# Optimization experiments

Measured on AMD Instinct MI355X. Metric: run time of the kernel, lower is better.

## Reference

```python
import jax, jax.numpy as jnp
import numpy as np

TEMPERATURE = 0.07
THRESHOLD = 0.7
NUM = 21          # config['data_loader']['args']['class_num']
EPS = 1e-12       # F.normalize eps
NEG_BIG = 1e30


def _nearest_down(x, H, W):
    # torch F.interpolate(mode='nearest'): in_idx = floor(out_idx * in/out)
    Hin, Win = x.shape[-2], x.shape[-1]
    ih = (jnp.arange(H) * Hin) // H
    iw = (jnp.arange(W) * Win) // W
    return x[..., ih[:, None], iw[None, :]]


def _l2n(x):
    return x / jnp.maximum(jnp.linalg.norm(x, axis=1, keepdims=True), EPS)


def setup_inputs() -> dict:
    key = jax.random.key(0)
    ks = jax.random.split(key, 6)
    B, C, H, W = 8, 256, 128, 128
    return {
        "labels": jax.random.randint(ks[0], (B, 512, 512), 0, NUM, dtype=jnp.int64)
        if jax.config.jax_enable_x64 else jax.random.randint(ks[0], (B, 512, 512), 0, NUM, dtype=jnp.int32),
        "features_old": jax.random.normal(ks[1], (B, C, H, W), dtype=jnp.float32),
        "features": jax.random.normal(ks[2], (B, C, H, W), dtype=jnp.float32),
        "outputs_old": jax.random.normal(ks[3], (B, 16, 512, 512), dtype=jnp.float32),
        "outputs": jax.random.normal(ks[4], (B, NUM, 512, 512), dtype=jnp.float32),
        "prototypes": jax.random.normal(ks[5], (NUM, C), dtype=jnp.float32),
        "num_class": 21,
        "num_old_class": 16,
        "num_new_class": 5,
        "epoch": 1,
        "train_step": 1,
        "len_epoch": 100,
    }


def reference(labels, features_old, features, outputs_old, outputs, prototypes,
              num_class, num_old_class, num_new_class, epoch, train_step, len_epoch):
    B, C, H, W = features.shape
    f32 = features.dtype

    # pseudo-label construction
    labels_down = _nearest_down(labels, H, W)                      # [B,H,W] int
    bgr_mask = (labels_down == 0).astype(labels_down.dtype)
    oo = jnp.where(outputs_old < THRESHOLD, 0.0, outputs_old)
    old_pred = jnp.argmax(oo, axis=1)                              # [B,512,512]
    old_down = _nearest_down(old_pred, H, W).astype(labels_down.dtype)
    pseudo = old_down * bgr_mask + labels_down                     # [B,H,W]
    lab = pseudo.reshape(-1)                                       # [N]
    mask = (lab >= 0) & (lab < NUM)

    # [N, C] normalized pixel features
    fa = _l2n(features.transpose(0, 2, 3, 1).reshape(-1, C))
    fo = _l2n(features_old.transpose(0, 2, 3, 1).reshape(-1, C))

    # per-class mean (segment reduce) replacing the python loop over unique labels
    seg = jnp.where(mask, lab, NUM)
    w = mask.astype(f32)
    counts = jax.ops.segment_sum(w, seg, num_segments=NUM + 1)[:NUM]          # [K]
    sum_a = jax.ops.segment_sum(fa * w[:, None], seg, num_segments=NUM + 1)[:NUM]
    sum_o = jax.ops.segment_sum(fo * w[:, None], seg, num_segments=NUM + 1)[:NUM]
    present = counts > 0
    denom = jnp.where(present, counts, 1.0)[:, None]
    anc = jnp.where(present[:, None], sum_a / denom, 0.0)          # [K,C] anchor prototypes
    con_prev = jnp.where(present[:, None], sum_o / denom, 0.0)     # [K,C] old prototypes
    contrast = jax.lax.stop_gradient(jnp.concatenate([anc, con_prev], axis=0))  # [2K,C]

    K = NUM
    eye = jnp.eye(K, dtype=f32)
    rowp = present.astype(f32)                                     # [K]
    colp = jnp.concatenate([rowp, rowp])                           # [2K]
    # labels are unique per row, so R = [I | I]; pos = [0 | I]; neg = 1 - R
    pos_mask = jnp.concatenate([jnp.zeros((K, K), f32), eye], axis=1) * rowp[:, None] * colp[None, :]
    neg_mask = (1.0 - jnp.concatenate([eye, eye], axis=1)) * rowp[:, None] * colp[None, :]

    adc = (anc @ contrast.T) / TEMPERATURE                         # [K,2K]
    # NOTE: faithful to source, negatives use UNshifted logits
    neg = jnp.sum(jnp.exp(adc) * neg_mask, axis=1, keepdims=True)  # [K,1]
    logits_max = jnp.max(jnp.where(colp[None, :] > 0, adc, -NEG_BIG), axis=1, keepdims=True)
    shifted = adc - jax.lax.stop_gradient(logits_max)
    pos_contrast = shifted * pos_mask - jnp.log(jnp.exp(shifted) + neg) * pos_mask

    num = pos_mask.sum(axis=1)
    valid = num > 0
    row_loss = -pos_contrast.sum(axis=1) / jnp.where(valid, num, 1.0)
    loss = jnp.sum(jnp.where(valid, row_loss, 0.0)) / jnp.maximum(jnp.sum(valid.astype(f32)), 1.0)
    return loss
```

## Files before the change

### kernel.cpp

```cpp
#include <hip/hip_runtime.h>
#include <math.h>

#define NPIX   131072
#define CCH    256
#define HW     16384
#define BSTR   4194304
#define NUMC   21
#define KC     5376
#define NREP   16

typedef __attribute__((ext_vector_type(8))) short bf16x8;
typedef __attribute__((ext_vector_type(4))) float f32x4;

static __device__ __forceinline__ uint f2bf(float x) {
    uint u = __builtin_bit_cast(uint, x);
    return (u + 0x7FFFu + ((u >> 16) & 1u)) >> 16;
}
static __device__ __forceinline__ uint ohv(int lbl, int cls, uint iv) {
    return (lbl == cls) ? iv : 0u;
}
static __device__ __forceinline__ float rsq_fast(float x) {
#if __has_builtin(__builtin_amdgcn_rsqf)
    return __builtin_amdgcn_rsqf(x);
#else
    return rsqrtf(x);
#endif
}
static __device__ __forceinline__ uint bfpack_trunc(float x, float y) {
    return __builtin_amdgcn_perm(__builtin_bit_cast(uint, y),
                                 __builtin_bit_cast(uint, x), 0x07060302u);
}

__global__ __launch_bounds__(256) void k_labels(const int* __restrict__ labels,
                                                const float* __restrict__ outputs_old,
                                                int* __restrict__ lab,
                                                float* __restrict__ gcnt)
{
    __shared__ float cnt[NUMC];
    if (threadIdx.x < NUMC) cnt[threadIdx.x] = 0.f;
    __syncthreads();

    int p = blockIdx.x * 256 + threadIdx.x;
    int b = p >> 14;
    int rem = p & 16383;
    int h = rem >> 7;
    int w = rem & 127;
    int ld = labels[b * 262144 + (h * 4) * 512 + (w * 4)];
    int out = ld;
    if (ld == 0) {
        const float* oo = outputs_old + (size_t)b * BSTR + (size_t)(h * 4) * 512 + (w * 4);
        float v0 = oo[0];
        float best = (v0 < 0.7f) ? 0.0f : v0;
        int bi = 0;
        #pragma unroll
        for (int c = 1; c < 16; ++c) {
            float v = oo[(size_t)c * 262144];
            v = (v < 0.7f) ? 0.0f : v;
            if (v > best) { best = v; bi = c; }
        }
        out = bi;
    }
    lab[p] = out;
    unsafeAtomicAdd(&cnt[out], 1.0f);
    __syncthreads();
    if (threadIdx.x < NUMC) unsafeAtomicAdd(&gcnt[threadIdx.x], cnt[threadIdx.x]);
}

__global__ __launch_bounds__(256, 2) void k_msum(const float* __restrict__ fa,
                                                 const float* __restrict__ fo,
                                                 const int* __restrict__ lab,
                                                 float* __restrict__ partA,
                                                 float* __restrict__ partO)
{
    __shared__ ushort tileB[CCH * 128];
    __shared__ float  ssqP[4][128];
    __shared__ float  invnS[128];
    __shared__ int    labS[256];

    const int t = threadIdx.x;
    const int w = t >> 6, l = t & 63;
    const int isO = blockIdx.x & 1;
    const float* __restrict__ src = isO ? fo : fa;
    float* part = isO ? partO : partA;

    const int pbase = (blockIdx.x >> 1) * 256;
    const int img   = pbase >> 14;
    const int hw0   = pbase & 16383;
    const float* g  = src + (size_t)img * BSTR + hw0;

    labS[t] = lab[pbase + t];

    f32x4 acc[2][4];
    #pragma unroll
    for (int m = 0; m < 2; ++m)
        #pragma unroll
        for (int n = 0; n < 4; ++n)
            acc[m][n] = (f32x4){0.f, 0.f, 0.f, 0.f};

#define LOADB(B, i0) do { \
    _Pragma("unroll") \
    for (int i_ = 0; i_ < 8; ++i_) \
        B[i_] = *(const float4*)(gc + (size_t)(w * 64 + 2 * ((i0) + i_) + (l >> 5)) * HW \
                                 + (l & 31) * 4); \
    } while (0)

#define PROCB(B, i0) do { \
    _Pragma("unroll") \
    for (int i_ = 0; i_ < 8; ++i_) { \
        float4 v_ = B[i_]; \
        s4.x += v_.x * v_.x;  s4.y += v_.y * v_.y; \
        s4.z += v_.z * v_.z;  s4.w += v_.w * v_.w; \
        int ch_ = w * 64 + 2 * ((i0) + i_) + (l >> 5); \
        uint lo_ = bfpack_trunc(v_.x, v_.y); \
        uint hi_ = bfpack_trunc(v_.z, v_.w); \
        *(uint2*)((char*)tileB + ch_ * 256 + ((((l & 31) * 8)) ^ ((ch_ & 7) << 4))) = \
            make_uint2(lo_, hi_); \
    } \
    } while (0)

#define KSTEP(c2, ks) do { \
    float4 ivA_ = *(const float4*)&invnS[(ks) * 32 + (l >> 4) * 8]; \
    float4 ivB_ = *(const float4*)&invnS[(ks) * 32 + (l >> 4) * 8 + 4]; \
    uint iv0 = f2bf(ivA_.x), iv1 = f2bf(ivA_.y), iv2 = f2bf(ivA_.z), iv3 = f2bf(ivA_.w); \
    uint iv4 = f2bf(ivB_.x), iv5 = f2bf(ivB_.y), iv6 = f2bf(ivB_.z), iv7 = f2bf(ivB_.w); \
    int4 la_ = *(const int4*)&labS[(c2) * 128 + (ks) * 32 + (l >> 4) * 8]; \
    int4 lb_ = *(const int4*)&labS[(c2) * 128 + (ks) * 32 + (l >> 4) * 8 + 4]; \
    const int cls0_ = l & 15, cls1_ = 16 + (l & 15); \
    uint4 u0_, u1_; \
    u0_.x = ohv(la_.x, cls0_, iv0) | (ohv(la_.y, cls0_, iv1) << 16); \
    u0_.y = ohv(la_.z, cls0_, iv2) | (ohv(la_.w, cls0_, iv3) << 16); \
    u0_.z = ohv(lb_.x, cls0_, iv4) | (ohv(lb_.y, cls0_, iv5) << 16); \
    u0_.w = ohv(lb_.z, cls0_, iv6) | (ohv(lb_.w, cls0_, iv7) << 16); \
    u1_.x = ohv(la_.x, cls1_, iv0) | (ohv(la_.y, cls1_, iv1) << 16); \
    u1_.y = ohv(la_.z, cls1_, iv2) | (ohv(la_.w, cls1_, iv3) << 16); \
    u1_.z = ohv(lb_.x, cls1_, iv4) | (ohv(lb_.y, cls1_, iv5) << 16); \
    u1_.w = ohv(lb_.z, cls1_, iv6) | (ohv(lb_.w, cls1_, iv7) << 16); \
    bf16x8 A0_ = __builtin_bit_cast(bf16x8, u0_); \
    bf16x8 A1_ = __builtin_bit_cast(bf16x8, u1_); \
    _Pragma("unroll") \
    for (int n_ = 0; n_ < 4; ++n_) { \
        const int chrow_ = (w * 4 + n_) * 16 + (l & 15); \
        const bf16x8 B_ = *(const bf16x8*)((const char*)tileB + chrow_ * 256 \
                            + (((ks) * 64 + (l >> 4) * 16) ^ ((chrow_ & 7) << 4))); \
        acc[0][n_] = __builtin_amdgcn_mfma_f32_16x16x32_bf16(A0_, B_, acc[0][n_], 0, 0, 0); \
        acc[1][n_] = __builtin_amdgcn_mfma_f32_16x16x32_bf16(A1_, B_, acc[1][n_], 0, 0, 0); \
    } \
    } while (0)

#define CHUNK(c2, LAST) do { \
    const float* gc = g + (c2) * 128; \
    float4 s4 = {0.f, 0.f, 0.f, 0.f}; \
    float4 bufA[8], bufB[8]; \
    LOADB(bufA, 0);  LOADB(bufB, 8); \
    PROCB(bufA, 0);  LOADB(bufA, 16); \
    PROCB(bufB, 8);  LOADB(bufB, 24); \
    PROCB(bufA, 16); PROCB(bufB, 24); \
    s4.x += __shfl_xor(s4.x, 32, 64);  s4.y += __shfl_xor(s4.y, 32, 64); \
    s4.z += __shfl_xor(s4.z, 32, 64);  s4.w += __shfl_xor(s4.w, 32, 64); \
    if (l < 32) *(float4*)&ssqP[w][l * 4] = s4; \
    __syncthreads(); \
    if (t < 128) { \
        float ss_ = ssqP[0][t] + ssqP[1][t] + ssqP[2][t] + ssqP[3][t]; \
        invnS[t] = rsq_fast(fmaxf(ss_, 1e-24f)); \
    } \
    __syncthreads(); \
    KSTEP(c2, 0); KSTEP(c2, 1); KSTEP(c2, 2); KSTEP(c2, 3); \
    if (!(LAST)) __syncthreads(); \
    } while (0)

    CHUNK(0, 0);
    CHUNK(1, 1);

#undef LOADB
#undef PROCB
#undef KSTEP
#undef CHUNK

    const int rep = (blockIdx.x >> 1) & (NREP - 1);
    #pragma unroll
    for (int m = 0; m < 2; ++m)
        #pragma unroll
        for (int n = 0; n < 4; ++n) {
            const int col = (w * 4 + n) * 16 + (l & 15);
            #pragma unroll
            for (int r = 0; r < 4; ++r) {
                const int row = m * 16 + (l >> 4) * 4 + r;
                if (row < NUMC)
                    unsafeAtomicAdd(&part[rep * KC + row * 256 + col], acc[m][n][r]);
            }
        }
}

__global__ __launch_bounds__(256) void k_red(const float* __restrict__ partA,
                                             const float* __restrict__ partO,
                                             float* __restrict__ gsum)
{
    const int b = blockIdx.x, t = threadIdx.x;
    const float* part = (b < 21) ? partA : partO;
    const int cls = (b < 21) ? b : b - 21;
    float s = 0.f;
    #pragma unroll
    for (int r = 0; r < NREP; ++r) s += part[r * KC + cls * 256 + t];
    gsum[b * 256 + t] = s;
}

__global__ __launch_bounds__(256) void k_final2(const float* __restrict__ gsum,
                                                const float* __restrict__ gcnt,
                                                float* __restrict__ out)
{
    __shared__ float anc[NUMC * 260];
    __shared__ float con[NUMC * 260];
    __shared__ float adc[NUMC * 44];
    __shared__ float cntS[NUMC];
    __shared__ float rowloss[NUMC];
    __shared__ float rowvalid[NUMC];

    if (threadIdx.x < NUMC) cntS[threadIdx.x] = gcnt[threadIdx.x];
    __syncthreads();
    for (int i = threadIdx.x; i < KC; i += 256) {
        int k = i >> 8, c = i & 255;
        float cn = cntS[k];
        bool pr = cn > 0.f;
        float d = pr ? cn : 1.f;
        anc[k * 260 + c] = pr ? gsum[k * 256 + c] / d : 0.f;
        con[k * 260 + c] = pr ? gsum[(NUMC + k) * 256 + c] / d : 0.f;
    }
    __syncthreads();
    for (int pair = threadIdx.x; pair < NUMC * 2 * NUMC; pair += 256) {
        int k = pair / (2 * NUMC);
        int j = pair % (2 * NUMC);
        const float* ar = anc + k * 260;
        const float* br = (j < NUMC) ? (anc + j * 260) : (con + (j - NUMC) * 260);
        float s = 0.f;
        for (int c = 0; c < CCH; c += 4) {
            float4 a4 = *(const float4*)(ar + c);
            float4 b4 = *(const float4*)(br + c);
            s += a4.x * b4.x + a4.y * b4.y + a4.z * b4.z + a4.w * b4.w;
        }
        adc[k * 44 + j] = s / 0.07f;
    }
    __syncthreads();
    if (threadIdx.x < NUMC) {
        int k = threadIdx.x;
        bool pr = cntS[k] > 0.f;
        float neg = 0.f;
        float mx = -1e30f;
        for (int j = 0; j < 2 * NUMC; ++j) {
            int cj = (j < NUMC) ? j : (j - NUMC);
            bool cp = cntS[cj] > 0.f;
            float v = adc[k * 44 + j];
            if (cp) {
                if (v > mx) mx = v;
                if (j != k && j != NUMC + k) neg += expf(v);
            }
        }
        float sh = adc[k * 44 + NUMC + k] - mx;
        float rl = -(sh - logf(expf(sh) + neg));
        rowloss[k] = pr ? rl : 0.f;
        rowvalid[k] = pr ? 1.f : 0.f;
    }
    __syncthreads();
    if (threadIdx.x == 0) {
        float s = 0.f, v = 0.f;
        for (int kk = 0; kk < NUMC; ++kk) { s += rowloss[kk]; v += rowvalid[kk]; }
        out[0] = s / fmaxf(v, 1.f);
    }
}

extern "C" void kernel_launch(void* const* d_in, const int* in_sizes, int n_in,
                              void* d_out, int out_size, void* d_ws, size_t ws_size,
                              hipStream_t stream) {
    const int*   labels      = (const int*)  d_in[0];
    const float* feats_old   = (const float*)d_in[1];
    const float* feats       = (const float*)d_in[2];
    const float* outputs_old = (const float*)d_in[3];

    float* ws    = (float*)d_ws;
    int*   lab   = (int*)ws;
    float* partA = ws + 131072;
    float* partO = partA + NREP * KC;
    float* gcnt  = partO + NREP * KC;
    float* gsum  = gcnt + 32;

    hipMemsetAsync(partA, 0, (size_t)(2 * NREP * KC + NUMC) * sizeof(float), stream);

    k_labels<<<NPIX / 256, 256, 0, stream>>>(labels, outputs_old, lab, gcnt);
    k_msum  <<<1024, 256, 0, stream>>>(feats, feats_old, lab, partA, partO);
    k_red   <<<42, 256, 0, stream>>>(partA, partO, gsum);
    k_final2<<<1, 256, 0, stream>>>(gsum, gcnt, (float*)d_out);
}
```

Before: 101.2 us.

## Process 512 pixels per k_msum block with cross-chunk prefetch and wider loads

Each k_msum block now covers 512 pixels, handled as two 256-pixel halves, and the grid is halved. Each wave loads a full 1 KB channel row per instruction, and the first loads of the second half are issued before the first half's norm and MFMA phase. This is meant to hide load latency and halve the atomic flushes into the partial buffers. In exchange the LDS tile doubles to 128 KB, which forces one block per CU and lowers occupancy. The bf16 packing also moves from truncation to round-to-nearest, which adds ALU work per element.

Measured after the change: 107.8 us. 6.5% more time.

```diff
diff --git a/kernel.cpp b/kernel.cpp
--- a/kernel.cpp
+++ b/kernel.cpp
@@ -25,10 +25,6 @@
 #else
     return rsqrtf(x);
 #endif
-}
-static __device__ __forceinline__ uint bfpack_trunc(float x, float y) {
-    return __builtin_amdgcn_perm(__builtin_bit_cast(uint, y),
-                                 __builtin_bit_cast(uint, x), 0x07060302u);
 }
 
 __global__ __launch_bounds__(256) void k_labels(const int* __restrict__ labels,
@@ -66,16 +62,16 @@
     if (threadIdx.x < NUMC) unsafeAtomicAdd(&gcnt[threadIdx.x], cnt[threadIdx.x]);
 }
 
-__global__ __launch_bounds__(256, 2) void k_msum(const float* __restrict__ fa,
+__global__ __launch_bounds__(256, 1) void k_msum(const float* __restrict__ fa,
                                                  const float* __restrict__ fo,
                                                  const int* __restrict__ lab,
                                                  float* __restrict__ partA,
                                                  float* __restrict__ partO)
 {
-    __shared__ ushort tileB[CCH * 128];
-    __shared__ float  ssqP[4][128];
-    __shared__ float  invnS[128];
-    __shared__ int    labS[256];
+    __shared__ ushort tileB[CCH * 256];
+    __shared__ float  ssqP[4][256];
+    __shared__ float  invnS[256];
+    __shared__ int    labS[512];
 
     const int t = threadIdx.x;
     const int w = t >> 6, l = t & 63;
@@ -83,12 +79,13 @@
     const float* __restrict__ src = isO ? fo : fa;
     float* part = isO ? partO : partA;
 
-    const int pbase = (blockIdx.x >> 1) * 256;
+    const int pbase = (blockIdx.x >> 1) * 512;
     const int img   = pbase >> 14;
     const int hw0   = pbase & 16383;
     const float* g  = src + (size_t)img * BSTR + hw0;
 
-    labS[t] = lab[pbase + t];
+    labS[t]       = lab[pbase + t];
+    labS[256 + t] = lab[pbase + 256 + t];
 
     f32x4 acc[2][4];
     #pragma unroll
@@ -97,34 +94,36 @@
         for (int n = 0; n < 4; ++n)
             acc[m][n] = (f32x4){0.f, 0.f, 0.f, 0.f};
 
-#define LOADB(B, i0) do { \
+#define SWZ(ch_) ((((ch_) & 15) << 4) ^ (((ch_) & 1) << 8))
+
+#define ISSUE(B, su, b) do { \
     _Pragma("unroll") \
     for (int i_ = 0; i_ < 8; ++i_) \
-        B[i_] = *(const float4*)(gc + (size_t)(w * 64 + 2 * ((i0) + i_) + (l >> 5)) * HW \
-                                 + (l & 31) * 4); \
+        B[i_] = *(const float4*)(g + (size_t)(w * 64 + (b) * 8 + i_) * HW \
+                                 + (su) * 256 + 4 * l); \
     } while (0)
 
-#define PROCB(B, i0) do { \
+#define PROC(B, b) do { \
     _Pragma("unroll") \
     for (int i_ = 0; i_ < 8; ++i_) { \
         float4 v_ = B[i_]; \
         s4.x += v_.x * v_.x;  s4.y += v_.y * v_.y; \
         s4.z += v_.z * v_.z;  s4.w += v_.w * v_.w; \
-        int ch_ = w * 64 + 2 * ((i0) + i_) + (l >> 5); \
-        uint lo_ = bfpack_trunc(v_.x, v_.y); \
-        uint hi_ = bfpack_trunc(v_.z, v_.w); \
-        *(uint2*)((char*)tileB + ch_ * 256 + ((((l & 31) * 8)) ^ ((ch_ & 7) << 4))) = \
+        int ch_ = w * 64 + (b) * 8 + i_; \
+        uint lo_ = f2bf(v_.x) | (f2bf(v_.y) << 16); \
+        uint hi_ = f2bf(v_.z) | (f2bf(v_.w) << 16); \
+        *(uint2*)((char*)tileB + ch_ * 512 + ((8 * l) ^ SWZ(ch_))) = \
             make_uint2(lo_, hi_); \
     } \
     } while (0)
 
-#define KSTEP(c2, ks) do { \
+#define KSTEP(su, ks) do { \
     float4 ivA_ = *(const float4*)&invnS[(ks) * 32 + (l >> 4) * 8]; \
     float4 ivB_ = *(const float4*)&invnS[(ks) * 32 + (l >> 4) * 8 + 4]; \
     uint iv0 = f2bf(ivA_.x), iv1 = f2bf(ivA_.y), iv2 = f2bf(ivA_.z), iv3 = f2bf(ivA_.w); \
     uint iv4 = f2bf(ivB_.x), iv5 = f2bf(ivB_.y), iv6 = f2bf(ivB_.z), iv7 = f2bf(ivB_.w); \
-    int4 la_ = *(const int4*)&labS[(c2) * 128 + (ks) * 32 + (l >> 4) * 8]; \
-    int4 lb_ = *(const int4*)&labS[(c2) * 128 + (ks) * 32 + (l >> 4) * 8 + 4]; \
+    int4 la_ = *(const int4*)&labS[(su) * 256 + (ks) * 32 + (l >> 4) * 8]; \
+    int4 lb_ = *(const int4*)&labS[(su) * 256 + (ks) * 32 + (l >> 4) * 8 + 4]; \
     const int cls0_ = l & 15, cls1_ = 16 + (l & 15); \
     uint4 u0_, u1_; \
     u0_.x = ohv(la_.x, cls0_, iv0) | (ohv(la_.y, cls0_, iv1) << 16); \
@@ -140,41 +139,58 @@
     _Pragma("unroll") \
     for (int n_ = 0; n_ < 4; ++n_) { \
         const int chrow_ = (w * 4 + n_) * 16 + (l & 15); \
-        const bf16x8 B_ = *(const bf16x8*)((const char*)tileB + chrow_ * 256 \
-                            + (((ks) * 64 + (l >> 4) * 16) ^ ((chrow_ & 7) << 4))); \
+        const bf16x8 B_ = *(const bf16x8*)((const char*)tileB + chrow_ * 512 \
+                            + (((ks) * 64 + (l >> 4) * 16) ^ SWZ(chrow_))); \
         acc[0][n_] = __builtin_amdgcn_mfma_f32_16x16x32_bf16(A0_, B_, acc[0][n_], 0, 0, 0); \
         acc[1][n_] = __builtin_amdgcn_mfma_f32_16x16x32_bf16(A1_, B_, acc[1][n_], 0, 0, 0); \
     } \
     } while (0)
 
-#define CHUNK(c2, LAST) do { \
-    const float* gc = g + (c2) * 128; \
-    float4 s4 = {0.f, 0.f, 0.f, 0.f}; \
-    float4 bufA[8], bufB[8]; \
-    LOADB(bufA, 0);  LOADB(bufB, 8); \
-    PROCB(bufA, 0);  LOADB(bufA, 16); \
-    PROCB(bufB, 8);  LOADB(bufB, 24); \
-    PROCB(bufA, 16); PROCB(bufB, 24); \
-    s4.x += __shfl_xor(s4.x, 32, 64);  s4.y += __shfl_xor(s4.y, 32, 64); \
-    s4.z += __shfl_xor(s4.z, 32, 64);  s4.w += __shfl_xor(s4.w, 32, 64); \
-    if (l < 32) *(float4*)&ssqP[w][l * 4] = s4; \
-    __syncthreads(); \
-    if (t < 128) { \
-        float ss_ = ssqP[0][t] + ssqP[1][t] + ssqP[2][t] + ssqP[3][t]; \
-        invnS[t] = rsq_fast(fmaxf(ss_, 1e-24f)); \
-    } \
-    __syncthreads(); \
-    KSTEP(c2, 0); KSTEP(c2, 1); KSTEP(c2, 2); KSTEP(c2, 3); \
-    if (!(LAST)) __syncthreads(); \
-    } while (0)
-
-    CHUNK(0, 0);
-    CHUNK(1, 1);
-
-#undef LOADB
-#undef PROCB
+    float4 bufA[8], bufB[8];
+    float4 s4 = {0.f, 0.f, 0.f, 0.f};
+
+    ISSUE(bufA, 0, 0);  ISSUE(bufB, 0, 1);
+    PROC(bufA, 0);  ISSUE(bufA, 0, 2);
+    PROC(bufB, 1);  ISSUE(bufB, 0, 3);
+    PROC(bufA, 2);  ISSUE(bufA, 0, 4);
+    PROC(bufB, 3);  ISSUE(bufB, 0, 5);
+    PROC(bufA, 4);  ISSUE(bufA, 0, 6);
+    PROC(bufB, 5);  ISSUE(bufB, 0, 7);
+    PROC(bufA, 6);
+    PROC(bufB, 7);
+    ISSUE(bufA, 1, 0);  ISSUE(bufB, 1, 1);
+
+    *(float4*)&ssqP[w][l * 4] = s4;
+    __syncthreads();
+    invnS[t] = rsq_fast(fmaxf(ssqP[0][t] + ssqP[1][t] + ssqP[2][t] + ssqP[3][t],
+                              1e-24f));
+    __syncthreads();
+    KSTEP(0, 0); KSTEP(0, 1); KSTEP(0, 2); KSTEP(0, 3);
+    KSTEP(0, 4); KSTEP(0, 5); KSTEP(0, 6); KSTEP(0, 7);
+    __syncthreads();
+
+    s4 = (float4){0.f, 0.f, 0.f, 0.f};
+    PROC(bufA, 0);  ISSUE(bufA, 1, 2);
+    PROC(bufB, 1);  ISSUE(bufB, 1, 3);
+    PROC(bufA, 2);  ISSUE(bufA, 1, 4);
+    PROC(bufB, 3);  ISSUE(bufB, 1, 5);
+    PROC(bufA, 4);  ISSUE(bufA, 1, 6);
+    PROC(bufB, 5);  ISSUE(bufB, 1, 7);
+    PROC(bufA, 6);
+    PROC(bufB, 7);
+
+    *(float4*)&ssqP[w][l * 4] = s4;
+    __syncthreads();
+    invnS[t] = rsq_fast(fmaxf(ssqP[0][t] + ssqP[1][t] + ssqP[2][t] + ssqP[3][t],
+                              1e-24f));
+    __syncthreads();
+    KSTEP(1, 0); KSTEP(1, 1); KSTEP(1, 2); KSTEP(1, 3);
+    KSTEP(1, 4); KSTEP(1, 5); KSTEP(1, 6); KSTEP(1, 7);
+
+#undef ISSUE
+#undef PROC
 #undef KSTEP
-#undef CHUNK
+#undef SWZ
 
     const int rep = (blockIdx.x >> 1) & (NREP - 1);
     #pragma unroll
@@ -285,7 +301,7 @@
     hipMemsetAsync(partA, 0, (size_t)(2 * NREP * KC + NUMC) * sizeof(float), stream);
 
     k_labels<<<NPIX / 256, 256, 0, stream>>>(labels, outputs_old, lab, gcnt);
-    k_msum  <<<1024, 256, 0, stream>>>(feats, feats_old, lab, partA, partO);
+    k_msum  <<<512, 256, 0, stream>>>(feats, feats_old, lab, partA, partO);
     k_red   <<<42, 256, 0, stream>>>(partA, partO, gsum);
     k_final2<<<1, 256, 0, stream>>>(gsum, gcnt, (float*)d_out);
 }
```
